# Kernel optimization log

Measured on AMD Instinct MI355X. Metric: run time of the kernel, lower is better.

Reference implementation:

```python
import jax, jax.numpy as jnp
import numpy as np

B, T, N, K = 1024, 4096, 2048, 16
M = 1 << K  # per-neuron memory size (use_hashing=False -> 2**k)


def setup_inputs() -> dict:
    key = jax.random.key(0)
    k1, k2, k3 = jax.random.split(key, 3)
    input_bits = jax.random.randint(k1, (B, T), 0, 2, dtype=jnp.int32)          # 0/1 bits
    connections = jax.random.randint(k2, (N, K), 0, T, dtype=jnp.int32)         # fixed wiring
    memory = jax.random.randint(k3, (N, M), 0, 256, dtype=jnp.int32)            # per-neuron RAM contents
    return {"input_bits": input_bits, "connections": connections, "memory": memory}


def reference(input_bits, connections, memory):
    # gather the k wired bits for every neuron: [B, N, K]
    gathered = input_bits[:, connections].astype(jnp.int32)
    # bit weights = powers of two (RAMNeuron._bit_weights), LSB-first
    bit_weights = (jnp.int32(1) << jnp.arange(K, dtype=jnp.int32))              # [K]
    # weighted sum -> memory address per (sample, neuron): [B, N]
    addresses = jnp.sum(gathered * bit_weights, axis=-1)
    # per-neuron memory lookup: memory[n, addresses[b, n]] -> [B, N]
    mems = memory[jnp.arange(N)[None, :], addresses]
    # output is the stored LSB as a bool bit
    return (mems & 1).astype(jnp.bool_)
```

## Files before the change

### kernel.cpp

```cpp
#include <hip/hip_runtime.h>
#include <cstdint>

#define Bc 1024
#define Tc 4096
#define Nc 2048
#define Kc 16
#define Mc 65536

#define PACK_GRID 2048
#define PACK_BLK  256

__global__ __launch_bounds__(PACK_BLK) void pack_bit0(
    const int* __restrict__ memory,
    unsigned long long* __restrict__ packed)
{
    const int tid  = threadIdx.x;
    const int lane = tid & 63;
    const size_t stride = (size_t)PACK_GRID * PACK_BLK;
    size_t base = (size_t)blockIdx.x * PACK_BLK + tid;

    for (int it = 0; it < 256 / 8; ++it) {
        int v[8];
#pragma unroll
        for (int j = 0; j < 8; ++j)
            v[j] = __builtin_nontemporal_load(memory + base + (size_t)j * stride);
#pragma unroll
        for (int j = 0; j < 8; ++j) {
            const unsigned long long m = __ballot(v[j] & 1);
            if (lane == 0) {
                packed[(base + (size_t)j * stride) >> 6] = m;
            }
        }
        base += 8 * stride;
    }
}

__global__ __launch_bounds__(256) void ram_lookup_packed(
    const int* __restrict__ input_bits,
    const int* __restrict__ connections,
    const uint32_t* __restrict__ packed,
    int* __restrict__ out)
{
    __shared__ uint32_t bits[Tc / 32];

    const int b    = blockIdx.x;
    const int tid  = threadIdx.x;
    const int lane = tid & 63;
    const int wave = tid >> 6;

    const int* row = input_bits + (size_t)b * Tc;

#pragma unroll
    for (int i = 0; i < Tc / 256; ++i) {
        const int pos = i * 256 + wave * 64 + lane;
        const unsigned long long m = __ballot(row[pos] & 1);
        if (lane == 0) {
            const int w64 = i * 4 + wave;
            bits[w64 * 2]     = (uint32_t)m;
            bits[w64 * 2 + 1] = (uint32_t)(m >> 32);
        }
    }
    __syncthreads();

    int vals[Nc / 256];
#pragma unroll
    for (int i = 0; i < Nc / 256; ++i) {
        const int n = i * 256 + tid;
        const int4* cp = (const int4*)(connections + n * Kc);
        const int4 c0 = cp[0], c1 = cp[1], c2 = cp[2], c3 = cp[3];
        const int c[16] = {c0.x, c0.y, c0.z, c0.w,
                           c1.x, c1.y, c1.z, c1.w,
                           c2.x, c2.y, c2.z, c2.w,
                           c3.x, c3.y, c3.z, c3.w};
        uint32_t a = 0;
#pragma unroll
        for (int k = 0; k < 16; ++k) {
            const uint32_t t = (uint32_t)c[k];
            a |= ((bits[t >> 5] >> (t & 31)) & 1u) << k;
        }
        const uint32_t w = packed[((uint32_t)n << 11) + (a >> 5)];
        vals[i] = (int)((w >> (a & 31)) & 1u);
    }

#pragma unroll
    for (int i = 0; i < Nc / 256; ++i) {
        __builtin_nontemporal_store(vals[i],
                                    out + (size_t)b * Nc + i * 256 + tid);
    }
}

__global__ __launch_bounds__(256) void ram_lookup_fused(
    const int* __restrict__ input_bits,
    const int* __restrict__ connections,
    const int* __restrict__ memory,
    int* __restrict__ out)
{
    __shared__ uint32_t bits[Tc / 32];

    const int b    = blockIdx.x;
    const int tid  = threadIdx.x;
    const int lane = tid & 63;
    const int wave = tid >> 6;

    const int* row = input_bits + (size_t)b * Tc;

#pragma unroll
    for (int i = 0; i < Tc / 256; ++i) {
        const int pos = i * 256 + wave * 64 + lane;
        const unsigned long long m = __ballot(row[pos] & 1);
        if (lane == 0) {
            const int w64 = i * 4 + wave;
            bits[w64 * 2]     = (uint32_t)m;
            bits[w64 * 2 + 1] = (uint32_t)(m >> 32);
        }
    }
    __syncthreads();

    int vals[Nc / 256];
#pragma unroll
    for (int i = 0; i < Nc / 256; ++i) {
        const int n = i * 256 + tid;
        const int4* cp = (const int4*)(connections + n * Kc);
        const int4 c0 = cp[0], c1 = cp[1], c2 = cp[2], c3 = cp[3];
        const int c[16] = {c0.x, c0.y, c0.z, c0.w,
                           c1.x, c1.y, c1.z, c1.w,
                           c2.x, c2.y, c2.z, c2.w,
                           c3.x, c3.y, c3.z, c3.w};
        uint32_t a = 0;
#pragma unroll
        for (int k = 0; k < 16; ++k) {
            const uint32_t t = (uint32_t)c[k];
            a |= ((bits[t >> 5] >> (t & 31)) & 1u) << k;
        }
        vals[i] = __builtin_nontemporal_load(memory + ((size_t)n << 16) + a);
    }

#pragma unroll
    for (int i = 0; i < Nc / 256; ++i) {
        __builtin_nontemporal_store(vals[i] & 1,
                                    out + (size_t)b * Nc + i * 256 + tid);
    }
}

extern "C" void kernel_launch(void* const* d_in, const int* in_sizes, int n_in,
                              void* d_out, int out_size, void* d_ws, size_t ws_size,
                              hipStream_t stream) {
    const int* input_bits  = (const int*)d_in[0];
    const int* connections = (const int*)d_in[1];
    const int* memory      = (const int*)d_in[2];
    int* out               = (int*)d_out;

    const size_t packed_bytes = (size_t)Nc * Mc / 8;

    if (ws_size >= packed_bytes) {
        unsigned long long* packed64 = (unsigned long long*)d_ws;
        hipLaunchKernelGGL(pack_bit0, dim3(PACK_GRID), dim3(PACK_BLK), 0, stream,
                           memory, packed64);
        hipLaunchKernelGGL(ram_lookup_packed, dim3(Bc), dim3(256), 0, stream,
                           input_bits, connections, (const uint32_t*)d_ws, out);
    } else {
        hipLaunchKernelGGL(ram_lookup_fused, dim3(Bc), dim3(256), 0, stream,
                           input_bits, connections, memory, out);
    }
}
```

Before: 737.3 us.

## Split into address kernel and per-neuron-group LDS bit-packed probe kernel

Replaces the global bit-packing pass plus scattered packed lookups. A first kernel computes all 16-bit addresses into workspace. A second kernel streams eight neurons' memory rows at a time, packs their LSBs into LDS with a permuted bit layout that matches the 128-bit loads, then serves every batch row's lookups from LDS. This removes the packed-table write and read round trip through global memory and the random global gathers. The cost is a 4 MB address buffer, 64 KB of LDS per block, and only 256 blocks, so occupancy is low.

```diff
diff --git a/kernel.cpp b/kernel.cpp
--- a/kernel.cpp
+++ b/kernel.cpp
@@ -7,39 +7,16 @@
 #define Kc 16
 #define Mc 65536
 
-#define PACK_GRID 2048
-#define PACK_BLK  256
+#define Gn 8
+#define GRID_B (Nc / Gn)
 
-__global__ __launch_bounds__(PACK_BLK) void pack_bit0(
-    const int* __restrict__ memory,
-    unsigned long long* __restrict__ packed)
-{
-    const int tid  = threadIdx.x;
-    const int lane = tid & 63;
-    const size_t stride = (size_t)PACK_GRID * PACK_BLK;
-    size_t base = (size_t)blockIdx.x * PACK_BLK + tid;
+typedef int  v4i  __attribute__((ext_vector_type(4)));
+typedef uint v4u  __attribute__((ext_vector_type(4)));
 
-    for (int it = 0; it < 256 / 8; ++it) {
-        int v[8];
-#pragma unroll
-        for (int j = 0; j < 8; ++j)
-            v[j] = __builtin_nontemporal_load(memory + base + (size_t)j * stride);
-#pragma unroll
-        for (int j = 0; j < 8; ++j) {
-            const unsigned long long m = __ballot(v[j] & 1);
-            if (lane == 0) {
-                packed[(base + (size_t)j * stride) >> 6] = m;
-            }
-        }
-        base += 8 * stride;
-    }
-}
-
-__global__ __launch_bounds__(256) void ram_lookup_packed(
+__global__ __launch_bounds__(256) void addr_kernel(
     const int* __restrict__ input_bits,
     const int* __restrict__ connections,
-    const uint32_t* __restrict__ packed,
-    int* __restrict__ out)
+    unsigned short* __restrict__ addr)
 {
     __shared__ uint32_t bits[Tc / 32];
 
@@ -62,7 +39,6 @@
     }
     __syncthreads();
 
-    int vals[Nc / 256];
 #pragma unroll
     for (int i = 0; i < Nc / 256; ++i) {
         const int n = i * 256 + tid;
@@ -78,14 +54,68 @@
             const uint32_t t = (uint32_t)c[k];
             a |= ((bits[t >> 5] >> (t & 31)) & 1u) << k;
         }
-        const uint32_t w = packed[((uint32_t)n << 11) + (a >> 5)];
-        vals[i] = (int)((w >> (a & 31)) & 1u);
+        addr[(size_t)b * Nc + n] = (unsigned short)a;
     }
+}
+
+__global__ __launch_bounds__(256) void probe_kernel(
+    const int* __restrict__ memory,
+    const unsigned short* __restrict__ addr,
+    int* __restrict__ out)
+{
+    __shared__ uint32_t prow[Gn][Mc / 32];
+
+    const int n0   = blockIdx.x * Gn;
+    const int tid  = threadIdx.x;
+    const int lane = tid & 63;
+    const int wave = tid >> 6;
+
+    for (int j = 0; j < 64; ++j) {
+        const int qb = wave * 512 + j * 8;
+        v4i v[8];
+#pragma unroll
+        for (int u = 0; u < 8; ++u) {
+            const int q = qb + u;
+            const int r = q >> 8;
+            const int it = q & 255;
+            v[u] = __builtin_nontemporal_load(
+                (const v4i*)(memory + (size_t)(n0 + r) * Mc) + it * 64 + lane);
+        }
+#pragma unroll
+        for (int u = 0; u < 8; ++u) {
+            const int q = qb + u;
+            const unsigned long long m0 = __ballot(v[u].x & 1);
+            const unsigned long long m1 = __ballot(v[u].y & 1);
+            const unsigned long long m2 = __ballot(v[u].z & 1);
+            const unsigned long long m3 = __ballot(v[u].w & 1);
+            if (lane < 8) {
+                const int c = lane >> 1;
+                const unsigned long long mm =
+                    (c == 0) ? m0 : (c == 1) ? m1 : (c == 2) ? m2 : m3;
+                prow[q >> 8][(q & 255) * 8 + lane] =
+                    (uint32_t)(mm >> ((lane & 1) << 5));
+            }
+        }
+    }
+    __syncthreads();
 
 #pragma unroll
-    for (int i = 0; i < Nc / 256; ++i) {
-        __builtin_nontemporal_store(vals[i],
-                                    out + (size_t)b * Nc + i * 256 + tid);
+    for (int j = 0; j < 4; ++j) {
+        const int b = j * 256 + tid;
+        const v4u av = *(const v4u*)(addr + (size_t)b * Nc + n0);
+        const uint32_t aw[4] = {av.x, av.y, av.z, av.w};
+        int res[8];
+#pragma unroll
+        for (int p = 0; p < 8; ++p) {
+            const uint32_t a   = (aw[p >> 1] >> ((p & 1) * 16)) & 0xffffu;
+            const uint32_t idx = ((a >> 8) << 3) + ((a & 3) << 1) + ((a >> 7) & 1);
+            res[p] = (int)((prow[p][idx] >> ((a >> 2) & 31)) & 1u);
+        }
+        v4i* op = (v4i*)(out + (size_t)b * Nc + n0);
+        v4i r0 = {res[0], res[1], res[2], res[3]};
+        v4i r1 = {res[4], res[5], res[6], res[7]};
+        __builtin_nontemporal_store(r0, op);
+        __builtin_nontemporal_store(r1, op + 1);
     }
 }
 
@@ -150,14 +180,14 @@
     const int* memory      = (const int*)d_in[2];
     int* out               = (int*)d_out;
 
-    const size_t packed_bytes = (size_t)Nc * Mc / 8;
+    const size_t addr_bytes = (size_t)Bc * Nc * sizeof(unsigned short);
 
-    if (ws_size >= packed_bytes) {
-        unsigned long long* packed64 = (unsigned long long*)d_ws;
-        hipLaunchKernelGGL(pack_bit0, dim3(PACK_GRID), dim3(PACK_BLK), 0, stream,
-                           memory, packed64);
-        hipLaunchKernelGGL(ram_lookup_packed, dim3(Bc), dim3(256), 0, stream,
-                           input_bits, connections, (const uint32_t*)d_ws, out);
+    if (ws_size >= addr_bytes) {
+        unsigned short* addr = (unsigned short*)d_ws;
+        hipLaunchKernelGGL(addr_kernel, dim3(Bc), dim3(256), 0, stream,
+                           input_bits, connections, addr);
+        hipLaunchKernelGGL(probe_kernel, dim3(GRID_B), dim3(256), 0, stream,
+                           memory, addr, out);
     } else {
         hipLaunchKernelGGL(ram_lookup_fused, dim3(Bc), dim3(256), 0, stream,
                            input_bits, connections, memory, out);
```

Result: faster. 675.1 us (-8.4%).

## Split lookup into address pass and LDS-staged per-neuron probe kernel

Applied to the files above, without the earlier changes.

Computes 16-bit addresses for every (sample, neuron) into a workspace buffer, then runs a probe kernel where each block stages the packed bit rows of 8 neurons into shared memory and answers all batch samples from it. This replaces scattered global reads into the packed bitmap with LDS lookups and vectorized output stores. It costs an extra kernel launch, a 4MB address round trip, and 64KB LDS per block, which limits occupancy; it also needs a larger workspace.

```diff
diff --git a/kernel.cpp b/kernel.cpp
--- a/kernel.cpp
+++ b/kernel.cpp
@@ -7,8 +7,14 @@
 #define Kc 16
 #define Mc 65536
 
+#define Gn 8
+#define GRID_B (Nc / Gn)
+
 #define PACK_GRID 2048
 #define PACK_BLK  256
+
+typedef int  v4i  __attribute__((ext_vector_type(4)));
+typedef uint v4u  __attribute__((ext_vector_type(4)));
 
 __global__ __launch_bounds__(PACK_BLK) void pack_bit0(
     const int* __restrict__ memory,
@@ -35,11 +41,10 @@
     }
 }
 
-__global__ __launch_bounds__(256) void ram_lookup_packed(
+__global__ __launch_bounds__(256) void addr_kernel(
     const int* __restrict__ input_bits,
     const int* __restrict__ connections,
-    const uint32_t* __restrict__ packed,
-    int* __restrict__ out)
+    unsigned short* __restrict__ addr)
 {
     __shared__ uint32_t bits[Tc / 32];
 
@@ -62,7 +67,6 @@
     }
     __syncthreads();
 
-    int vals[Nc / 256];
 #pragma unroll
     for (int i = 0; i < Nc / 256; ++i) {
         const int n = i * 256 + tid;
@@ -78,14 +82,50 @@
             const uint32_t t = (uint32_t)c[k];
             a |= ((bits[t >> 5] >> (t & 31)) & 1u) << k;
         }
-        const uint32_t w = packed[((uint32_t)n << 11) + (a >> 5)];
-        vals[i] = (int)((w >> (a & 31)) & 1u);
-    }
-
-#pragma unroll
-    for (int i = 0; i < Nc / 256; ++i) {
-        __builtin_nontemporal_store(vals[i],
-                                    out + (size_t)b * Nc + i * 256 + tid);
+        addr[(size_t)b * Nc + n] = (unsigned short)a;
+    }
+}
+
+__global__ __launch_bounds__(256) void probe_kernel(
+    const uint32_t* __restrict__ packed32,
+    const unsigned short* __restrict__ addr,
+    int* __restrict__ out)
+{
+    __shared__ uint32_t prow[Gn * 2048];
+
+    const int n0  = blockIdx.x * Gn;
+    const int tid = threadIdx.x;
+
+    const v4u* src = (const v4u*)(packed32 + (size_t)n0 * 2048);
+#pragma unroll
+    for (int i = 0; i < 16; ++i) {
+        const int w = i * 256 + tid;
+        const v4u x = src[w];
+        *(v4u*)&prow[w * 4] = x;
+    }
+    __syncthreads();
+
+    v4u av[4];
+#pragma unroll
+    for (int j = 0; j < 4; ++j) {
+        const int b = j * 256 + tid;
+        av[j] = *(const v4u*)(addr + (size_t)b * Nc + n0);
+    }
+#pragma unroll
+    for (int j = 0; j < 4; ++j) {
+        const int b = j * 256 + tid;
+        const uint32_t aw[4] = {av[j].x, av[j].y, av[j].z, av[j].w};
+        int res[8];
+#pragma unroll
+        for (int p = 0; p < 8; ++p) {
+            const uint32_t a = (aw[p >> 1] >> ((p & 1) * 16)) & 0xffffu;
+            res[p] = (int)((prow[p * 2048 + (a >> 5)] >> (a & 31)) & 1u);
+        }
+        v4i* op = (v4i*)(out + (size_t)b * Nc + n0);
+        v4i r0 = {res[0], res[1], res[2], res[3]};
+        v4i r1 = {res[4], res[5], res[6], res[7]};
+        __builtin_nontemporal_store(r0, op);
+        __builtin_nontemporal_store(r1, op + 1);
     }
 }
 
@@ -150,14 +190,19 @@
     const int* memory      = (const int*)d_in[2];
     int* out               = (int*)d_out;
 
+    const size_t addr_bytes   = (size_t)Bc * Nc * sizeof(unsigned short);
     const size_t packed_bytes = (size_t)Nc * Mc / 8;
 
-    if (ws_size >= packed_bytes) {
-        unsigned long long* packed64 = (unsigned long long*)d_ws;
+    if (ws_size >= addr_bytes + packed_bytes) {
+        unsigned short* addr     = (unsigned short*)d_ws;
+        unsigned long long* pk64 = (unsigned long long*)((char*)d_ws + addr_bytes);
+
         hipLaunchKernelGGL(pack_bit0, dim3(PACK_GRID), dim3(PACK_BLK), 0, stream,
-                           memory, packed64);
-        hipLaunchKernelGGL(ram_lookup_packed, dim3(Bc), dim3(256), 0, stream,
-                           input_bits, connections, (const uint32_t*)d_ws, out);
+                           memory, pk64);
+        hipLaunchKernelGGL(addr_kernel, dim3(Bc), dim3(256), 0, stream,
+                           input_bits, connections, addr);
+        hipLaunchKernelGGL(probe_kernel, dim3(GRID_B), dim3(256), 0, stream,
+                           (const uint32_t*)pk64, addr, out);
     } else {
         hipLaunchKernelGGL(ram_lookup_fused, dim3(Bc), dim3(256), 0, stream,
                            input_bits, connections, memory, out);
```

Result: no change. 746.3 us (+1.2%).
